# Performance work log

Hardware: AMD Instinct MI355X
Metric: run time of the kernel (lower is better)

## Reference

```python
import jax, jax.numpy as jnp
import numpy as np

B, IMG, TXT, N, FF, HID, C, E = 1024, 512, 300, 14, 2048, 128, 14, 182
D = IMG + TXT  # 812, transformer d_model


def setup_inputs() -> dict:
    key = jax.random.key(0)
    ks = jax.random.split(key, 12)
    r = lambda k, s, sc=0.02: (jax.random.normal(k, s, jnp.float32) * sc)
    return {
        "img_feat": jax.random.normal(ks[0], (B, IMG), jnp.float32),
        "word_embeds": jax.random.normal(ks[1], (N, TXT), jnp.float32),
        "edge_index": jax.random.randint(ks[2], (2, E), 0, N, jnp.int32),
        "in_proj_w": r(ks[3], (3 * D, D)),
        "in_proj_b": jnp.zeros((3 * D,), jnp.float32),
        "out_proj_w": r(ks[4], (D, D)),
        "out_proj_b": jnp.zeros((D,), jnp.float32),
        "ln1_g": jnp.ones((D,), jnp.float32), "ln1_b": jnp.zeros((D,), jnp.float32),
        "ln2_g": jnp.ones((D,), jnp.float32), "ln2_b": jnp.zeros((D,), jnp.float32),
        "ffn_w1": r(ks[5], (D, FF)), "ffn_b1": jnp.zeros((FF,), jnp.float32),
        "ffn_w2": r(ks[6], (FF, D)), "ffn_b2": jnp.zeros((D,), jnp.float32),
        "gcn1_w": r(ks[7], (D, HID)), "gcn1_b": jnp.zeros((HID,), jnp.float32),
        "gcn2_w": r(ks[8], (HID, HID)), "gcn2_b": jnp.zeros((HID,), jnp.float32),
        "lin_w": r(ks[9], (HID, C)), "lin_b": jnp.zeros((C,), jnp.float32),
    }


def layer_norm(x, g, b, eps=1e-5):
    mu = x.mean(-1, keepdims=True)
    var = ((x - mu) ** 2).mean(-1, keepdims=True)
    return (x - mu) * jax.lax.rsqrt(var + eps) * g + b


def gcn_conv(x, edge_index, W, b, n_nodes):
    # PyG GCNConv: add self loops, symmetric normalization, x @ W then scatter-add.
    # x: (B, N, F_in); gather/scatter along node axis (node_dim=-2).
    src, dst = edge_index[0], edge_index[1]
    loop = jnp.arange(n_nodes, dtype=src.dtype)
    src = jnp.concatenate([src, loop])
    dst = jnp.concatenate([dst, loop])
    deg = jnp.zeros((n_nodes,), x.dtype).at[dst].add(1.0)
    dinv = jnp.where(deg > 0, deg ** -0.5, 0.0)
    ew = dinv[src] * dinv[dst]                       # (E+N,)
    h = x @ W                                        # (B, N, F_out)
    msg = h[:, src, :] * ew[None, :, None]           # gather neighbors
    out = jnp.zeros_like(h).at[:, dst, :].add(msg)   # scatter-aggregate
    return out + b


def reference(img_feat, word_embeds, edge_index,
              in_proj_w, in_proj_b, out_proj_w, out_proj_b,
              ln1_g, ln1_b, ln2_g, ln2_b,
              ffn_w1, ffn_b1, ffn_w2, ffn_b2,
              gcn1_w, gcn1_b, gcn2_w, gcn2_b, lin_w, lin_b):
    # Broadcast image feature across the 14 label nodes; concat word embeddings.
    node = jnp.concatenate([
        jnp.broadcast_to(img_feat[:, None, :], (B, N, IMG)),
        jnp.broadcast_to(word_embeds[None, :, :], (B, N, TXT)),
    ], axis=-1)                                      # (B, N, D)

    # torch TransformerEncoderLayer, batch_first=False, nhead=1, post-norm, relu.
    # Input (B, N, D) is interpreted as (seq=B, batch=N, D): attention over dim 0.
    qkv = node @ in_proj_w.T + in_proj_b
    q, k, v = jnp.split(qkv, 3, axis=-1)             # each (B, N, D)
    scale = 1.0 / jnp.sqrt(jnp.asarray(D, node.dtype))
    scores = jnp.einsum('lnd,mnd->nlm', q, k) * scale  # (N, B, B)
    attn = jax.nn.softmax(scores, axis=-1)
    ao = jnp.einsum('nlm,mnd->lnd', attn, v)           # (B, N, D)
    ao = ao @ out_proj_w.T + out_proj_b
    x = layer_norm(node + ao, ln1_g, ln1_b)
    ff = jax.nn.relu(x @ ffn_w1 + ffn_b1) @ ffn_w2 + ffn_b2
    x = layer_norm(x + ff, ln2_g, ln2_b)               # (B, N, D)

    # Two GCNConv layers over the 14-node label graph (batched over B).
    x = jax.nn.relu(gcn_conv(x, edge_index, gcn1_w, gcn1_b, N))
    x = gcn_conv(x, edge_index, gcn2_w, gcn2_b, N)
    x = jax.nn.relu(x.mean(axis=1))                    # mean over nodes -> (B, HID)
    return x @ lin_w + lin_b                           # (B, C)
```

## Files before the change

### kernel.cpp

```cpp
#include <hip/hip_runtime.h>
#include <math.h>

#define B_    1024
#define IMG_  512
#define TXT_  300
#define NN_   14
#define FF_   2048
#define HID_  128
#define CC_   14
#define EE_   182
#define DD_   812
#define D3_   2436
#define BNR_  14336
#define KP_   832
#define TXP_  320
#define AROWS_ 1152

typedef __bf16 bf16x8 __attribute__((ext_vector_type(8)));
typedef float  f32x4  __attribute__((ext_vector_type(4)));
typedef unsigned short u16;

__device__ __forceinline__ u16 f2bf(float f) {
    union { float f; unsigned u; } v; v.f = f;
    unsigned r = v.u + 0x7FFFu + ((v.u >> 16) & 1u);
    return (u16)(r >> 16);
}
__device__ __forceinline__ float bf2f(u16 h) {
    union { unsigned u; float f; } v; v.u = ((unsigned)h) << 16; return v.f;
}

__device__ __forceinline__ void gload_lds16(const u16* g, u16* l) {
    __builtin_amdgcn_global_load_lds(
        (const __attribute__((address_space(1))) void*)g,
        (__attribute__((address_space(3))) void*)l, 16, 0, 0);
}

#define OFF_IMGB  0ULL
#define OFF_WIB   1048576ULL
#define OFF_WORDB 3543040ULL
#define OFF_WITX  3624960ULL
#define OFF_GB    0ULL
#define OFF_EBUF  29360128ULL
#define OFF_AVOT  33611776ULL
#define OFF_WOB   35446784ULL
#define OFF_HB    0ULL
#define OFF_PB    58720256ULL
#define OFF_X1B   82001920ULL
#define OFF_YB    105857024ULL
#define OFF_W1T   129712128ULL
#define OFF_W2T   133120000ULL
#define OFF_AQB   152420352ULL
#define OFF_TVB   158307552ULL
#define OFF_CO    158520544ULL
#define OFF_Z     158566016ULL
#define OFF_ADJ   158623360ULL
#define OFF_WG1T  158624384ULL
#define OFF_WG2T  158837376ULL

__device__ __forceinline__ void gemm_epi(
    float v, int rm, int cn, int epi,
    float* __restrict__ Cf, int ldc, u16* __restrict__ Cb, int ldcb,
    const float* __restrict__ bias)
{
    if (epi == 0) Cf[(size_t)rm * ldc + cn] = v;
    else if (epi == 1) { v += bias[cn]; v = v > 0.f ? v : 0.f;
                    Cb[(size_t)rm * ldcb + cn] = f2bf(v); }
    else if (epi == 2) Cf[(size_t)rm * ldc + cn] =
                    v + bias[cn] + bf2f(Cb[(size_t)rm * ldcb + cn]);
    else if (epi == 3) Cb[(size_t)rm * ldcb + cn] = f2bf(v);
    else if (epi == 4) { int bs = cn / DD_, cc = cn - bs * DD_;
                    Cb[(size_t)bs * (AROWS_ * KP_) + (size_t)rm * KP_ + cc] = f2bf(v); }
    else if (epi == 5) { float invz = 1.0f / bias[rm];
                    Cb[(size_t)rm * ldcb + cn] = f2bf(v * invz); }
    else if (epi == 6) Cf[(size_t)rm * ldc + cn] = v + bias[cn];
    else if (epi == 7) { const u16* rx = (const u16*)Cf;
                    Cb[(size_t)rm * ldcb + cn] =
                        f2bf(v + bias[cn] + bf2f(rx[(size_t)rm * ldc + cn])); }
    else if (epi == 8) {
        float t = v + bias[cn];
        if (cn < DD_) Cb[(size_t)(1024 + rm) * KP_ + cn] = f2bf(t);
        else if (cn >= 2 * DD_)
            ((u16*)Cf)[(size_t)rm * KP_ + (cn - 2 * DD_)] = f2bf(t);
    }
}

__device__ __forceinline__ void gemm_body4(
    const u16* __restrict__ A, int lda,
    const u16* __restrict__ Bm, int ldb,
    int M, int N, int K, float scale,
    float* __restrict__ Cf, int ldc,
    u16* __restrict__ Cb, int ldcb,
    const float* __restrict__ bias,
    int nxt, int swiz, int epi, int id)
{
    __shared__ __align__(16) u16 As[2][128 * 32];
    __shared__ __align__(16) u16 Bs[2][128 * 32];
    const int tid = threadIdx.x;
    int bx, by;
    if (swiz) { int r8 = id & 7; int q = id >> 3; bx = q % nxt; by = (q / nxt) * 8 + r8; }
    else      { bx = id % nxt; by = id / nxt; }
    const int row0 = by * 128, col0 = bx * 128;
    const int lane = tid & 63, wv = tid >> 6;
    const int wm = (wv >> 1) * 64, wn = (wv & 1) * 64;
    const int fr = lane & 15, qd = lane >> 4;

    const int s_r0  = (wv * 64 + lane) >> 2;
    const int s_sw  = ((lane & 3) ^ ((lane >> 3) & 3)) * 8;
    const int s_b0  = (wv * 64) * 8;
    const u16* Arow0 = A  + (size_t)(row0 + s_r0) * lda + s_sw;
    const u16* Arow1 = A  + (size_t)(row0 + s_r0 + 64) * lda + s_sw;
    const u16* Brow0 = Bm + (size_t)(col0 + s_r0) * ldb + s_sw;
    const u16* Brow1 = Bm + (size_t)(col0 + s_r0 + 64) * ldb + s_sw;
    const int qsw = (qd ^ ((fr >> 1) & 3)) * 8;

    f32x4 acc[4][4] = {};

    const int T = K >> 5;
    gload_lds16(Arow0, &As[0][s_b0]);
    gload_lds16(Arow1, &As[0][s_b0 + 2048]);
    gload_lds16(Brow0, &Bs[0][s_b0]);
    gload_lds16(Brow1, &Bs[0][s_b0 + 2048]);

    for (int i = 0; i < T; ++i) {
        __syncthreads();
        const int cur = i & 1;
        if (i + 1 < T) {
            const int nb = cur ^ 1;
            const int ko = (i + 1) << 5;
            gload_lds16(Arow0 + ko, &As[nb][s_b0]);
            gload_lds16(Arow1 + ko, &As[nb][s_b0 + 2048]);
            gload_lds16(Brow0 + ko, &Bs[nb][s_b0]);
            gload_lds16(Brow1 + ko, &Bs[nb][s_b0 + 2048]);
        }
        bf16x8 af[4], bg[4];
        #pragma unroll
        for (int j = 0; j < 4; ++j) {
            af[j] = *(const bf16x8*)&As[cur][(wm + j * 16 + fr) * 32 + qsw];
            bg[j] = *(const bf16x8*)&Bs[cur][(wn + j * 16 + fr) * 32 + qsw];
        }
        #pragma unroll
        for (int mi = 0; mi < 4; ++mi)
            #pragma unroll
            for (int ni = 0; ni < 4; ++ni)
                acc[mi][ni] = __builtin_amdgcn_mfma_f32_16x16x32_bf16(
                    af[mi], bg[ni], acc[mi][ni], 0, 0, 0);
    }

    #pragma unroll
    for (int mi = 0; mi < 4; ++mi) {
        #pragma unroll
        for (int i = 0; i < 4; ++i) {
            int rm = row0 + wm + mi * 16 + qd * 4 + i;
            if (rm >= M) continue;
            #pragma unroll
            for (int ni = 0; ni < 4; ++ni) {
                int cn = col0 + wn + ni * 16 + fr;
                if (cn >= N) continue;
                gemm_epi(acc[mi][ni][i] * scale, rm, cn, epi, Cf, ldc, Cb, ldcb, bias);
            }
        }
    }
}

template<int EPI>
__global__ __launch_bounds__(256, 4)
void bgemm(const u16* __restrict__ A, int lda,
           const u16* __restrict__ Bm, int ldb,
           int M, int N, int K, float scale,
           float* __restrict__ Cf, int ldc,
           u16* __restrict__ Cb, int ldcb,
           const float* __restrict__ bias,
           int nxt, int swiz)
{
    gemm_body4(A, lda, Bm, ldb, M, N, K, scale, Cf, ldc, Cb, ldcb, bias,
               nxt, swiz, EPI, blockIdx.x);
}

__device__ __forceinline__ void gemm256_body(
    const u16* __restrict__ A, int lda,
    const u16* __restrict__ Bm, int ldb,
    int M, int N, int K, float scale,
    float* __restrict__ Cf, int ldc,
    u16* __restrict__ Cb, int ldcb,
    const float* __restrict__ bias,
    int nxt, int epi, int id)
{
    __shared__ __align__(16) u16 As[4][8192];
    __shared__ __align__(16) u16 Bs[4][8192];
    const int tid = threadIdx.x;
    const int bx = id % nxt, by = id / nxt;
    const int row0 = by << 8, col0 = bx << 8;
    const int lane = tid & 63, wv = tid >> 6;
    const int wm = (wv >> 2) << 7;
    const int wn = (wv & 3) << 6;
    const int fr = lane & 15, qd = lane >> 4;

    int aoff[8], boff[4];
    #pragma unroll
    for (int mi = 0; mi < 8; ++mi) {
        int r = wm + mi * 16 + fr;
        aoff[mi] = r * 32 + ((qd ^ ((r >> 1) & 3)) << 3);
    }
    #pragma unroll
    for (int ni = 0; ni < 4; ++ni) {
        int r = wn + ni * 16 + fr;
        boff[ni] = r * 32 + ((qd ^ ((r >> 1) & 3)) << 3);
    }

    const int i0 = tid, i1 = 512 + tid;
    const int r0 = i0 >> 2, r1 = i1 >> 2;
    const int c0 = ((i0 & 3) ^ ((r0 >> 1) & 3)) << 3;
    const int c1 = ((i1 & 3) ^ ((r1 >> 1) & 3)) << 3;
    const u16* Ag0 = A  + (size_t)(row0 + r0) * lda + c0;
    const u16* Ag1 = A  + (size_t)(row0 + r1) * lda + c1;
    const u16* Bg0 = Bm + (size_t)(col0 + r0) * ldb + c0;
    const u16* Bg1 = Bm + (size_t)(col0 + r1) * ldb + c1;
    const int lb0 = wv * 512;
    const int lb1 = 4096 + wv * 512;

    f32x4 acc[8][4] = {};
    const int T = K >> 5;

    #pragma unroll
    for (int p = 0; p < 3; ++p) {
        const int ko = p << 5;
        gload_lds16(Ag0 + ko, &As[p][lb0]);
        gload_lds16(Ag1 + ko, &As[p][lb1]);
        gload_lds16(Bg0 + ko, &Bs[p][lb0]);
        gload_lds16(Bg1 + ko, &Bs[p][lb1]);
    }
    __builtin_amdgcn_sched_barrier(0);
    asm volatile("s_waitcnt vmcnt(8)");
    __builtin_amdgcn_sched_barrier(0);
    __builtin_amdgcn_s_barrier();
    __builtin_amdgcn_sched_barrier(0);

    for (int t = 0; t < T; ++t) {
        const int slot = t & 3;
        const u16* as = &As[slot][0];
        const u16* bs = &Bs[slot][0];
        const int ns = (t + 3) & 3;
        const int ko = (t + 3) << 5;
        const bool pf = (t + 3 < T);

        bf16x8 a[8];
        #pragma unroll
        for (int mi = 0; mi < 8; ++mi)
            a[mi] = *(const bf16x8*)(as + aoff[mi]);
        bf16x8 b0 = *(const bf16x8*)(bs + boff[0]);
        bf16x8 b1 = *(const bf16x8*)(bs + boff[1]);
        if (pf) {
            gload_lds16(Ag0 + ko, &As[ns][lb0]);
            gload_lds16(Ag1 + ko, &As[ns][lb1]);
        }
        __builtin_amdgcn_sched_barrier(0);
        __builtin_amdgcn_s_barrier();
        __builtin_amdgcn_sched_barrier(0);
        __builtin_amdgcn_s_setprio(1);
        #pragma unroll
        for (int mi = 0; mi < 8; ++mi) {
            acc[mi][0] = __builtin_amdgcn_mfma_f32_16x16x32_bf16(
                a[mi], b0, acc[mi][0], 0, 0, 0);
            acc[mi][1] = __builtin_amdgcn_mfma_f32_16x16x32_bf16(
                a[mi], b1, acc[mi][1], 0, 0, 0);
        }
        __builtin_amdgcn_s_setprio(0);
        __builtin_amdgcn_sched_barrier(0);
        __builtin_amdgcn_s_barrier();
        __builtin_amdgcn_sched_barrier(0);

        bf16x8 b2 = *(const bf16x8*)(bs + boff[2]);
        bf16x8 b3 = *(const bf16x8*)(bs + boff[3]);
        if (pf) {
            gload_lds16(Bg0 + ko, &Bs[ns][lb0]);
            gload_lds16(Bg1 + ko, &Bs[ns][lb1]);
        }
        __builtin_amdgcn_sched_barrier(0);
        if (t < T - 3) asm volatile("s_waitcnt vmcnt(8)");
        else           asm volatile("s_waitcnt vmcnt(0)");
        __builtin_amdgcn_sched_barrier(0);
        __builtin_amdgcn_s_barrier();
        __builtin_amdgcn_sched_barrier(0);
        __builtin_amdgcn_s_setprio(1);
        #pragma unroll
        for (int mi = 0; mi < 8; ++mi) {
            acc[mi][2] = __builtin_amdgcn_mfma_f32_16x16x32_bf16(
                a[mi], b2, acc[mi][2], 0, 0, 0);
            acc[mi][3] = __builtin_amdgcn_mfma_f32_16x16x32_bf16(
                a[mi], b3, acc[mi][3], 0, 0, 0);
        }
        __builtin_amdgcn_s_setprio(0);
        __builtin_amdgcn_sched_barrier(0);
        __builtin_amdgcn_s_barrier();
        __builtin_amdgcn_sched_barrier(0);
    }

    #pragma unroll
    for (int mi = 0; mi < 8; ++mi) {
        #pragma unroll
        for (int i = 0; i < 4; ++i) {
            int rm = row0 + wm + mi * 16 + qd * 4 + i;
            if (rm >= M) continue;
            #pragma unroll
            for (int ni = 0; ni < 4; ++ni) {
                int cn = col0 + wn + ni * 16 + fr;
                if (cn >= N) continue;
                gemm_epi(acc[mi][ni][i] * scale, rm, cn, epi, Cf, ldc, Cb, ldcb, bias);
            }
        }
    }
}

template<int EPI>
__global__ __launch_bounds__(512, 2)
void bgemm256(const u16* __restrict__ A, int lda,
              const u16* __restrict__ Bm, int ldb,
              int M, int N, int K, float scale,
              float* __restrict__ Cf, int ldc,
              u16* __restrict__ Cb, int ldcb,
              const float* __restrict__ bias,
              int nxt)
{
    const int g8 = (int)gridDim.x >> 3;
    const int id = (int)blockIdx.x;
    const int w = (id & 7) * g8 + (id >> 3);
    gemm256_body(A, lda, Bm, ldb, M, N, K, scale, Cf, ldc, Cb, ldcb, bias,
                 nxt, EPI, w);
}

__device__ __forceinline__ void gemm_body8(
    const u16* __restrict__ A, int lda,
    const u16* __restrict__ Bm, int ldb,
    int M, int N, int K, float scale,
    float* __restrict__ Cf, int ldc,
    u16* __restrict__ Cb, int ldcb,
    const float* __restrict__ bias,
    int nxt, int swiz, int epi, int id)
{
    __shared__ __align__(16) u16 As[2][128 * 32];
    __shared__ __align__(16) u16 Bs[2][128 * 32];
    const int tid = threadIdx.x;
    int bx, by;
    if (swiz) { int r8 = id & 7; int q = id >> 3; bx = q % nxt; by = (q / nxt) * 8 + r8; }
    else      { bx = id % nxt; by = id / nxt; }
    const int row0 = by * 128, col0 = bx * 128;
    const int lane = tid & 63, wv = tid >> 6;
    const int wm = (wv >> 1) * 32, wn = (wv & 1) * 64;
    const int fr = lane & 15, qd = lane >> 4;

    const int s_b0  = wv * 512;
    const int s_row = tid >> 2;
    const int s_sw  = ((tid & 3) ^ ((tid >> 3) & 3)) * 8;
    const u16* Arow = A  + (size_t)(row0 + s_row) * lda + s_sw;
    const u16* Brow = Bm + (size_t)(col0 + s_row) * ldb + s_sw;
    const int qsw = (qd ^ ((fr >> 1) & 3)) * 8;

    f32x4 acc[2][4] = {};

    const int T = K >> 5;
    gload_lds16(Arow, &As[0][s_b0]);
    gload_lds16(Brow, &Bs[0][s_b0]);

    for (int i = 0; i < T; ++i) {
        __syncthreads();
        const int cur = i & 1;
        if (i + 1 < T) {
            const int ko = (i + 1) << 5;
            gload_lds16(Arow + ko, &As[cur ^ 1][s_b0]);
            gload_lds16(Brow + ko, &Bs[cur ^ 1][s_b0]);
        }
        bf16x8 af[2], bg[4];
        #pragma unroll
        for (int j = 0; j < 2; ++j)
            af[j] = *(const bf16x8*)&As[cur][(wm + j * 16 + fr) * 32 + qsw];
        #pragma unroll
        for (int j = 0; j < 4; ++j)
            bg[j] = *(const bf16x8*)&Bs[cur][(wn + j * 16 + fr) * 32 + qsw];
        #pragma unroll
        for (int mi = 0; mi < 2; ++mi)
            #pragma unroll
            for (int ni = 0; ni < 4; ++ni)
                acc[mi][ni] = __builtin_amdgcn_mfma_f32_16x16x32_bf16(
                    af[mi], bg[ni], acc[mi][ni], 0, 0, 0);
    }

    #pragma unroll
    for (int mi = 0; mi < 2; ++mi) {
        #pragma unroll
        for (int i = 0; i < 4; ++i) {
            int rm = row0 + wm + mi * 16 + qd * 4 + i;
            if (rm >= M) continue;
            #pragma unroll
            for (int ni = 0; ni < 4; ++ni) {
                int cn = col0 + wn + ni * 16 + fr;
                if (cn >= N) continue;
                gemm_epi(acc[mi][ni][i] * scale, rm, cn, epi, Cf, ldc, Cb, ldcb, bias);
            }
        }
    }
}

struct GDesc {
    const u16* A; const u16* B; float* Cf; u16* Cb; const float* bias;
    int lda, ldb, ldc, ldcb, M, N, K, epi, nxt, swiz, blk0;
    float scale;
};
struct TDesc { const float* src; u16* dst; int srs, drs, rows, cols, padrows, rt, nblk; };
struct MPack { GDesc g[3]; TDesc t[2]; const int* ei; float* Adj; int ng, gtot, nt; };

__device__ __forceinline__ void castT_body(TDesc T, int id)
{
    __shared__ float t[32][33];
    const int bx = id % T.rt, by = id / T.rt;
    const int r0 = bx * 32, c0 = by * 32;
    const int tx = threadIdx.x & 31, ty = threadIdx.x >> 5;
    #pragma unroll
    for (int k = 0; k < 2; ++k) {
        int r = r0 + ty + k * 16, c = c0 + tx;
        t[ty + k * 16][tx] = (r < T.rows && c < T.cols) ? T.src[(size_t)r * T.srs + c] : 0.f;
    }
    __syncthreads();
    #pragma unroll
    for (int k = 0; k < 2; ++k) {
        int c = c0 + ty + k * 16, r = r0 + tx;
        if (c < T.cols && r < T.padrows)
            T.dst[(size_t)c * T.drs + r] = f2bf(t[tx][ty + k * 16]);
    }
}

__device__ __forceinline__ void adj_body(const int* __restrict__ ei, float* __restrict__ Adj)
{
    __shared__ float degS[NN_], dinvS[NN_], adjS[NN_ * NN_];
    const int tid = threadIdx.x;
    if (tid < NN_) degS[tid] = 1.f;
    if (tid < NN_ * NN_) adjS[tid] = 0.f;
    __syncthreads();
    int s = 0, d = 0;
    if (tid < EE_) { s = ei[tid]; d = ei[EE_ + tid]; atomicAdd(&degS[d], 1.f); }
    __syncthreads();
    if (tid < NN_) dinvS[tid] = rsqrtf(degS[tid]);
    __syncthreads();
    if (tid < EE_) atomicAdd(&adjS[d * NN_ + s], dinvS[s] * dinvS[d]);
    if (tid < NN_) atomicAdd(&adjS[tid * NN_ + tid], dinvS[tid] * dinvS[tid]);
    __syncthreads();
    if (tid < NN_ * NN_) Adj[tid] = adjS[tid];
    if (tid < 16) {
        float sum = 0.f;
        if (tid < NN_)
            for (int j = 0; j < NN_; ++j) sum += adjS[j * NN_ + tid];
        Adj[NN_ * NN_ + tid] = sum / (float)NN_;
    }
}

__global__ __launch_bounds__(512, 6)
void kern_mix(MPack p)
{
    int id = blockIdx.x;
    if (id < p.gtot) {
        int si = 0;
        for (int s = 1; s < p.ng; ++s) if (id >= p.g[s].blk0) si = s;
        GDesc D = p.g[si];
        gemm_body8(D.A, D.lda, D.B, D.ldb, D.M, D.N, D.K, D.scale,
                   D.Cf, D.ldc, D.Cb, D.ldcb, D.bias, D.nxt, D.swiz, D.epi,
                   id - D.blk0);
        return;
    }
    id -= p.gtot;
    for (int s = 0; s < p.nt; ++s) {
        if (id < p.t[s].nblk) { castT_body(p.t[s], id); return; }
        id -= p.t[s].nblk;
    }
    if (id == 0 && p.ei) adj_body(p.ei, p.Adj);
}

struct CDesc { const float* src; u16* dst; int srs, drs, dcols, scols; };
struct CPack { CDesc d[9]; unsigned cum[10]; int n; };

__global__ void kern_mcast(CPack p)
{
    unsigned idx = blockIdx.x * 256 + threadIdx.x;
    int si = -1;
    for (int s = 0; s < p.n; ++s)
        if (idx >= p.cum[s] && idx < p.cum[s + 1]) { si = s; break; }
    if (si < 0) return;
    CDesc D = p.d[si];
    unsigned k = idx - p.cum[si];
    int r = k / D.dcols, c = k - r * D.dcols;
    D.dst[(size_t)r * D.drs + c] =
        (c < D.scols) ? f2bf(D.src[(size_t)r * D.srs + c]) : (u16)0;
}

__global__ __launch_bounds__(256) void kern_eG(const float* __restrict__ S,
    u16* __restrict__ Gb, float* __restrict__ Z)
{
    __shared__ float red[256];
    __shared__ u16 ews[NN_ * 1024];
    const int l = blockIdx.x, tid = threadIdx.x;
    const int lane = tid & 63, wv = tid >> 6;

    const float* wraw = S + 1024 * 1024;
    for (int z = wv; z < NN_; z += 4) {
        const float* r = wraw + z * 1024;
        float vv[16], mx = -1e30f;
        #pragma unroll
        for (int j = 0; j < 16; ++j) { vv[j] = r[lane + 64 * j]; mx = fmaxf(mx, vv[j]); }
        #pragma unroll
        for (int off = 32; off > 0; off >>= 1) mx = fmaxf(mx, __shfl_down(mx, off));
        mx = __shfl(mx, 0);
        #pragma unroll
        for (int j = 0; j < 16; ++j)
            ews[z * 1024 + lane + 64 * j] = f2bf(expf(vv[j] - mx));
    }
    const float* row = S + (size_t)l * 1024;
    float m = -1e30f;
    #pragma unroll
    for (int k = 0; k < 4; ++k) m = fmaxf(m, row[tid + 256 * k]);
    red[tid] = m; __syncthreads();
    for (int s = 128; s > 0; s >>= 1) {
        if (tid < s) red[tid] = fmaxf(red[tid], red[tid + s]);
        __syncthreads();
    }
    m = red[0];
    float ev[16];
    #pragma unroll
    for (int j = 0; j < 16; ++j) ev[j] = expf(row[lane + 64 * j] - m);
    u16* gr = Gb + (size_t)l * NN_ * 1024;
    for (int z = wv; z < NN_; z += 4) {
        const u16* er = &ews[z * 1024];
        float s = 0.f;
        #pragma unroll
        for (int j = 0; j < 16; ++j) {
            float pv = ev[j] * bf2f(er[lane + 64 * j]);
            gr[(size_t)z * 1024 + lane + 64 * j] = f2bf(pv);
            s += pv;
        }
        #pragma unroll
        for (int off = 32; off > 0; off >>= 1) s += __shfl_down(s, off);
        if (lane == 0) Z[l * NN_ + z] = s;
    }
}

__global__ __launch_bounds__(256) void kern_ln1(
    const float* __restrict__ img, const float* __restrict__ word,
    const u16* __restrict__ Pb,
    const float* __restrict__ co, const float* __restrict__ g,
    const float* __restrict__ bta, u16* __restrict__ Xb)
{
    __shared__ float buf[DD_];
    __shared__ float red[256];
    __shared__ float stats[2];
    int row = blockIdx.x;
    int b = row / NN_, n = row - b * NN_;
    const u16* pr = Pb + (size_t)row * DD_;
    const float* cr = co + n * DD_;
    float s = 0.f;
    for (int d = threadIdx.x; d < DD_; d += 256) {
        float v = (d < IMG_) ? img[(size_t)b * IMG_ + d] : word[n * TXT_ + d - IMG_];
        v += bf2f(pr[d]) + cr[d];
        buf[d] = v; s += v;
    }
    red[threadIdx.x] = s; __syncthreads();
    for (int t = 128; t > 0; t >>= 1) {
        if (threadIdx.x < t) red[threadIdx.x] += red[threadIdx.x + t];
        __syncthreads();
    }
    if (threadIdx.x == 0) stats[0] = red[0] / DD_;
    __syncthreads();
    float mu = stats[0], s2 = 0.f;
    for (int d = threadIdx.x; d < DD_; d += 256) { float t = buf[d] - mu; s2 += t * t; }
    red[threadIdx.x] = s2; __syncthreads();
    for (int t = 128; t > 0; t >>= 1) {
        if (threadIdx.x < t) red[threadIdx.x] += red[threadIdx.x + t];
        __syncthreads();
    }
    if (threadIdx.x == 0) stats[1] = rsqrtf(red[0] / DD_ + 1e-5f);
    __syncthreads();
    float rstd = stats[1];
    u16* xb = Xb + (size_t)row * KP_;
    for (int d = threadIdx.x; d < DD_; d += 256)
        xb[d] = f2bf((buf[d] - mu) * rstd * g[d] + bta[d]);
    for (int d = DD_ + threadIdx.x; d < KP_; d += 256) xb[d] = 0;
}

#define X2S_ 840
#define G1S_ 136
__global__ __launch_bounds__(256, 4)
void kern_gcn(const u16* __restrict__ Yb,
              const float* __restrict__ g2v, const float* __restrict__ bt2,
              const u16* __restrict__ Wg1T, const float* __restrict__ bg1,
              const u16* __restrict__ Wg2T, const float* __restrict__ bg2,
              const float* __restrict__ Wl,  const float* __restrict__ bl,
              const float* __restrict__ AdjW, float* __restrict__ out)
{
    __shared__ __align__(16) u16 x2s[16 * X2S_];
    __shared__ __align__(16) float h1s[16 * 132];
    __shared__ float adj_s[NN_ * NN_];
    __shared__ float colw_s[16];
    __shared__ float pool_s[HID_];
    u16* g1s = x2s;
    const int b = blockIdx.x, tid = threadIdx.x;
    const int lane = tid & 63, wv = tid >> 6;
    const int fr = lane & 15, qd = lane >> 4;

    if (tid < NN_ * NN_) adj_s[tid] = AdjW[tid];
    if (tid >= NN_ * NN_ && tid < NN_ * NN_ + 16) colw_s[tid - NN_ * NN_] = AdjW[tid];
    for (int k = tid; k < 2 * X2S_; k += 256) x2s[14 * X2S_ + k] = 0;
    for (int k = tid; k < 14 * (X2S_ - DD_); k += 256) {
        int j = k / (X2S_ - DD_), c = k - j * (X2S_ - DD_);
        x2s[j * X2S_ + DD_ + c] = 0;
    }

    for (int j = wv; j < NN_; j += 4) {
        const u16* yr = Yb + (size_t)(b * NN_ + j) * KP_;
        float vv[13], s = 0.f;
        #pragma unroll
        for (int k = 0; k < 13; ++k) {
            int d = lane + 64 * k;
            float v = (d < DD_) ? bf2f(yr[d]) : 0.f;
            vv[k] = v; s += v;
        }
        #pragma unroll
        for (int off = 32; off > 0; off >>= 1) s += __shfl_down(s, off);
        s = __shfl(s, 0);
        float mu = s / (float)DD_, s2 = 0.f;
        #pragma unroll
        for (int k = 0; k < 13; ++k) {
            int d = lane + 64 * k;
            float t = (d < DD_) ? vv[k] - mu : 0.f;
            s2 += t * t;
        }
        #pragma unroll
        for (int off = 32; off > 0; off >>= 1) s2 += __shfl_down(s2, off);
        s2 = __shfl(s2, 0);
        float rstd = rsqrtf(s2 / (float)DD_ + 1e-5f);
        #pragma unroll
        for (int k = 0; k < 13; ++k) {
            int d = lane + 64 * k;
            if (d < DD_)
                x2s[j * X2S_ + d] = f2bf((vv[k] - mu) * rstd * g2v[d] + bt2[d]);
        }
    }
    __syncthreads();

    {
        f32x4 acc[2] = {{}, {}};
        const u16* wp0 = Wg1T + (size_t)(wv * 32 + fr) * KP_ + qd * 8;
        const u16* wp1 = wp0 + (size_t)16 * KP_;
        bf16x8 bc0 = *(const bf16x8*)wp0;
        bf16x8 bc1 = *(const bf16x8*)wp1;
        for (int k0 = 0; k0 < KP_; k0 += 32) {
            bf16x8 bn0 = bc0, bn1 = bc1;
            if (k0 + 32 < KP_) {
                bn0 = *(const bf16x8*)(wp0 + k0 + 32);
                bn1 = *(const bf16x8*)(wp1 + k0 + 32);
            }
            bf16x8 af = *(const bf16x8*)&x2s[fr * X2S_ + k0 + qd * 8];
            acc[0] = __builtin_amdgcn_mfma_f32_16x16x32_bf16(af, bc0, acc[0], 0, 0, 0);
            acc[1] = __builtin_amdgcn_mfma_f32_16x16x32_bf16(af, bc1, acc[1], 0, 0, 0);
            bc0 = bn0; bc1 = bn1;
        }
        #pragma unroll
        for (int t = 0; t < 2; ++t)
            #pragma unroll
            for (int i = 0; i < 4; ++i)
                h1s[(qd * 4 + i) * 132 + wv * 32 + t * 16 + fr] = acc[t][i];
    }
    __syncthreads();

    {
        const int f = tid & 127, jj = (tid >> 7) * 7;
        #pragma unroll
        for (int j = 0; j < 7; ++j) {
            float s = bg1[f];
            #pragma unroll
            for (int i = 0; i < NN_; ++i)
                s = fmaf(adj_s[(jj + j) * NN_ + i], h1s[i * 132 + f], s);
            g1s[(jj + j) * G1S_ + f] = f2bf(s > 0.f ? s : 0.f);
        }
        for (int k = tid; k < 2 * G1S_; k += 256) g1s[14 * G1S_ + k] = 0;
    }
    __syncthreads();

    {
        f32x4 acc[2] = {{}, {}};
        const u16* wp0 = Wg2T + (size_t)(wv * 32 + fr) * HID_ + qd * 8;
        const u16* wp1 = wp0 + (size_t)16 * HID_;
        bf16x8 bc0 = *(const bf16x8*)wp0;
        bf16x8 bc1 = *(const bf16x8*)wp1;
        for (int k0 = 0; k0 < HID_; k0 += 32) {
            bf16x8 bn0 = bc0, bn1 = bc1;
            if (k0 + 32 < HID_) {
                bn0 = *(const bf16x8*)(wp0 + k0 + 32);
                bn1 = *(const bf16x8*)(wp1 + k0 + 32);
            }
            bf16x8 af = *(const bf16x8*)&g1s[fr * G1S_ + k0 + qd * 8];
            acc[0] = __builtin_amdgcn_mfma_f32_16x16x32_bf16(af, bc0, acc[0], 0, 0, 0);
            acc[1] = __builtin_amdgcn_mfma_f32_16x16x32_bf16(af, bc1, acc[1], 0, 0, 0);
            bc0 = bn0; bc1 = bn1;
        }
        #pragma unroll
        for (int t = 0; t < 2; ++t) {
            float s = 0.f;
            #pragma unroll
            for (int i = 0; i < 4; ++i) s += colw_s[qd * 4 + i] * acc[t][i];
            s += __shfl_xor(s, 16);
            s += __shfl_xor(s, 32);
            if (qd == 0) {
                int f = wv * 32 + t * 16 + fr;
                float p = s + bg2[f];
                pool_s[f] = p > 0.f ? p : 0.f;
            }
        }
    }
    __syncthreads();

    if (tid < CC_) {
        float s = bl[tid];
        #pragma unroll 8
        for (int f = 0; f < HID_; ++f)
            s = fmaf(pool_s[f], Wl[(size_t)f * CC_ + tid], s);
        out[(size_t)b * CC_ + tid] = s;
    }
}

extern "C" void kernel_launch(void* const* d_in, const int* in_sizes, int n_in,
                              void* d_out, int out_size, void* d_ws, size_t ws_size,
                              hipStream_t stream)
{
    const float* img  = (const float*)d_in[0];
    const float* word = (const float*)d_in[1];
    const int*   ei   = (const int*)d_in[2];
    const float* Wi   = (const float*)d_in[3];
    const float* bi   = (const float*)d_in[4];
    const float* Wo   = (const float*)d_in[5];
    const float* bo   = (const float*)d_in[6];
    const float* g1   = (const float*)d_in[7];
    const float* bt1  = (const float*)d_in[8];
    const float* g2   = (const float*)d_in[9];
    const float* bt2  = (const float*)d_in[10];
    const float* W1   = (const float*)d_in[11];
    const float* bf1  = (const float*)d_in[12];
    const float* W2   = (const float*)d_in[13];
    const float* bf2  = (const float*)d_in[14];
    const float* Wg1  = (const float*)d_in[15];
    const float* bg1  = (const float*)d_in[16];
    const float* Wg2  = (const float*)d_in[17];
    const float* bg2  = (const float*)d_in[18];
    const float* Wl   = (const float*)d_in[19];
    const float* bl   = (const float*)d_in[20];
    float* out = (float*)d_out;

    char* ws = (char*)d_ws;
    u16*   imgb = (u16*)  (ws + OFF_IMGB);
    u16*   Wib  = (u16*)  (ws + OFF_WIB);
    u16*   wordb= (u16*)  (ws + OFF_WORDB);
    u16*   WiTX = (u16*)  (ws + OFF_WITX);
    u16*   Gb   = (u16*)  (ws + OFF_GB);
    float* Ebuf = (float*)(ws + OFF_EBUF);
    u16*   AvoT = (u16*)  (ws + OFF_AVOT);
    u16*   Wob  = (u16*)  (ws + OFF_WOB);
    u16*   Hb   = (u16*)  (ws + OFF_HB);
    u16*   Pb   = (u16*)  (ws + OFF_PB);
    u16*   X1b  = (u16*)  (ws + OFF_X1B);
    u16*   Yb   = (u16*)  (ws + OFF_YB);
    u16*   W1T  = (u16*)  (ws + OFF_W1T);
    u16*   W2T  = (u16*)  (ws + OFF_W2T);
    u16*   Aqb  = (u16*)  (ws + OFF_AQB);
    u16*   Akb  = Aqb + AROWS_ * KP_;
    u16*   Avb  = Aqb + 2 * AROWS_ * KP_;
    u16*   Tvb  = (u16*)  (ws + OFF_TVB);
    float* co   = (float*)(ws + OFF_CO);
    float* Zb   = (float*)(ws + OFF_Z);
    float* Adj  = (float*)(ws + OFF_ADJ);
    u16*   Wg1T = (u16*)  (ws + OFF_WG1T);
    u16*   Wg2T = (u16*)  (ws + OFF_WG2T);

    const float scl = 1.0f / sqrtf((float)DD_);

    {
        CPack p; p.n = 9;
        unsigned c = 0;
        auto seg = [&](int i, const float* s, int srs, u16* d, int drs,
                       int rows, int dcols, int scols) {
            p.d[i] = { s, d, srs, drs, dcols, scols };
            p.cum[i] = c; c += (unsigned)rows * dcols;
        };
        seg(0, img,        IMG_, imgb,  IMG_, B_,   IMG_, IMG_);
        seg(1, Wi,         DD_,  Wib,   IMG_, D3_,  IMG_, IMG_);
        seg(2, word,       TXT_, wordb, TXP_, NN_,  TXP_, TXT_);
        seg(3, Wi + IMG_,  DD_,  WiTX,  TXP_, D3_,  TXP_, TXT_);
        seg(4, Wo,         DD_,  Wob,   KP_,  DD_,  KP_,  DD_);
        seg(5, nullptr, 0, Aqb + DD_,                    KP_, 1038, 20, 0);
        seg(6, nullptr, 0, Aqb + AROWS_ * KP_ + DD_,     KP_, 1024, 20, 0);
        seg(7, nullptr, 0, Aqb + 2 * AROWS_ * KP_ + DD_, KP_, 1024, 20, 0);
        seg(8, nullptr, 0, Tvb + DD_,                    KP_, NN_,  20, 0);
        p.cum[9] = c;
        kern_mcast<<<(c + 255) / 256, 256, 0, stream>>>(p);
    }

    {
        MPack p{};
        p.ng = 2; p.gtot = 180;
        p.g[0] = { wordb, WiTX, (float*)Tvb, Aqb, bi,
                   TXP_, TXP_, 0, 0, NN_, D3_, TXP_, 8, 20, 0, 0, 1.f };
        p.g[1] = { imgb, Wib, nullptr, Aqb, nullptr,
                   IMG_, IMG_, 0, 0, B_, D3_, IMG_, 4, 20, 1, 20, 1.f };
        p.nt = 2;
        p.t[0] = { Wg1, Wg1T, HID_, KP_,  DD_,  HID_, KP_,  26, 26 * 4 };
        p.t[1] = { Wg2, Wg2T, HID_, HID_, HID_, HID_, HID_, 4,  4 * 4 };
        p.ei = ei; p.Adj = Adj;
        kern_mix<<<180 + 104 + 16 + 1, 512, 0, stream>>>(p);
    }

    {
        MPack p{};
        p.ng = 3; p.gtot = 135;
        p.g[0] = { Aqb, Akb, Ebuf, nullptr, nullptr,
                   KP_, KP_, 1024, 0, 1024 + NN_, 1024, KP_, 0, 8, 0, 0, scl };
        p.g[1] = { Wob, Avb, nullptr, AvoT, nullptr,
                   KP_, KP_, 0, 1024, DD_, B_, KP_, 3, 8, 0, 72, 1.f };
        p.g[2] = { Tvb, Wob, co, nullptr, bo,
                   KP_, KP_, DD_, 0, NN_, DD_, KP_, 6, 7, 0, 128, 1.f };
        p.nt = 2;
        p.t[0] = { W1, W1T, FF_, KP_, DD_, FF_, KP_, 26, 26 * 64 };
        p.t[1] = { W2, W2T, DD_, FF_, FF_, DD_, FF_, 64, 64 * 26 };
        p.ei = nullptr; p.Adj = nullptr;
        kern_mix<<<135 + 1664 + 1664, 512, 0, stream>>>(p);
    }

    kern_eG<<<1024, 256, 0, stream>>>(Ebuf, Gb, Zb);

    bgemm<5><<<7 * 112, 256, 0, stream>>>(Gb, 1024, AvoT, 1024,
        BNR_, DD_, 1024, 1.f, nullptr, 0, Pb, DD_, Zb, 7, 1);

    kern_ln1<<<BNR_, 256, 0, stream>>>(img, word, Pb, co, g1, bt1, X1b);

    bgemm<1><<<16 * 112, 256, 0, stream>>>(X1b, KP_, W1T, KP_,
        BNR_, FF_, KP_, 1.f, nullptr, 0, Hb, FF_, bf1, 16, 1);

    bgemm256<7><<<56 * 4, 512, 0, stream>>>(Hb, FF_, W2T, FF_,
        BNR_, DD_, FF_, 1.f, (float*)X1b, KP_, Yb, KP_, bf2, 4);

    kern_gcn<<<B_, 256, 0, stream>>>(Yb, g2, bt2, Wg1T, bg1, Wg2T, bg2,
                                     Wl, bl, Adj, out);
}
```

Baseline: 457.4 us.

## Split-K across warp groups in mixed GEMM and vectorize LN1 kernel

```diff
diff --git a/kernel.cpp b/kernel.cpp
--- a/kernel.cpp
+++ b/kernel.cpp
@@ -19,6 +19,8 @@
 typedef __bf16 bf16x8 __attribute__((ext_vector_type(8)));
 typedef float  f32x4  __attribute__((ext_vector_type(4)));
 typedef unsigned short u16;
+typedef unsigned short u16x4 __attribute__((ext_vector_type(4)));
+typedef unsigned short u16x8 __attribute__((ext_vector_type(8)));
 
 __device__ __forceinline__ u16 f2bf(float f) {
     union { float f; unsigned u; } v; v.f = f;
@@ -337,64 +339,88 @@
     const float* __restrict__ bias,
     int nxt, int swiz, int epi, int id)
 {
-    __shared__ __align__(16) u16 As[2][128 * 32];
-    __shared__ __align__(16) u16 Bs[2][128 * 32];
+    __shared__ __align__(16) u16 As[2][2][128 * 32];
+    __shared__ __align__(16) u16 Bs[2][2][128 * 32];
     const int tid = threadIdx.x;
     int bx, by;
     if (swiz) { int r8 = id & 7; int q = id >> 3; bx = q % nxt; by = (q / nxt) * 8 + r8; }
     else      { bx = id % nxt; by = id / nxt; }
     const int row0 = by * 128, col0 = bx * 128;
     const int lane = tid & 63, wv = tid >> 6;
-    const int wm = (wv >> 1) * 32, wn = (wv & 1) * 64;
+    const int kg = wv >> 2;
+    const int ww = wv & 3;
+    const int wm = (ww >> 1) * 64, wn = (ww & 1) * 64;
     const int fr = lane & 15, qd = lane >> 4;
 
-    const int s_b0  = wv * 512;
-    const int s_row = tid >> 2;
-    const int s_sw  = ((tid & 3) ^ ((tid >> 3) & 3)) * 8;
-    const u16* Arow = A  + (size_t)(row0 + s_row) * lda + s_sw;
-    const u16* Brow = Bm + (size_t)(col0 + s_row) * ldb + s_sw;
+    const int r0   = ww * 16 + (lane >> 2);
+    const int s_sw = ((lane & 3) ^ ((lane >> 3) & 3)) * 8;
+    const u16* Ag0 = A  + (size_t)(row0 + r0) * lda + s_sw;
+    const u16* Ag1 = A  + (size_t)(row0 + r0 + 64) * lda + s_sw;
+    const u16* Bg0 = Bm + (size_t)(col0 + r0) * ldb + s_sw;
+    const u16* Bg1 = Bm + (size_t)(col0 + r0 + 64) * ldb + s_sw;
+    const int lb0 = ww * 512, lb1 = 2048 + ww * 512;
     const int qsw = (qd ^ ((fr >> 1) & 3)) * 8;
 
-    f32x4 acc[2][4] = {};
-
-    const int T = K >> 5;
-    gload_lds16(Arow, &As[0][s_b0]);
-    gload_lds16(Brow, &Bs[0][s_b0]);
-
-    for (int i = 0; i < T; ++i) {
+    f32x4 acc[4][4] = {};
+    const int Th = K >> 6;
+    const int kb = kg * Th;
+
+    gload_lds16(Ag0 + (kb << 5), &As[kg][0][lb0]);
+    gload_lds16(Ag1 + (kb << 5), &As[kg][0][lb1]);
+    gload_lds16(Bg0 + (kb << 5), &Bs[kg][0][lb0]);
+    gload_lds16(Bg1 + (kb << 5), &Bs[kg][0][lb1]);
+
+    for (int i = 0; i < Th; ++i) {
         __syncthreads();
         const int cur = i & 1;
-        if (i + 1 < T) {
-            const int ko = (i + 1) << 5;
-            gload_lds16(Arow + ko, &As[cur ^ 1][s_b0]);
-            gload_lds16(Brow + ko, &Bs[cur ^ 1][s_b0]);
-        }
-        bf16x8 af[2], bg[4];
-        #pragma unroll
-        for (int j = 0; j < 2; ++j)
-            af[j] = *(const bf16x8*)&As[cur][(wm + j * 16 + fr) * 32 + qsw];
-        #pragma unroll
-        for (int j = 0; j < 4; ++j)
-            bg[j] = *(const bf16x8*)&Bs[cur][(wn + j * 16 + fr) * 32 + qsw];
-        #pragma unroll
-        for (int mi = 0; mi < 2; ++mi)
+        if (i + 1 < Th) {
+            const int ko = (kb + i + 1) << 5;
+            gload_lds16(Ag0 + ko, &As[kg][cur ^ 1][lb0]);
+            gload_lds16(Ag1 + ko, &As[kg][cur ^ 1][lb1]);
+            gload_lds16(Bg0 + ko, &Bs[kg][cur ^ 1][lb0]);
+            gload_lds16(Bg1 + ko, &Bs[kg][cur ^ 1][lb1]);
+        }
+        bf16x8 af[4], bg[4];
+        #pragma unroll
+        for (int j = 0; j < 4; ++j) {
+            af[j] = *(const bf16x8*)&As[kg][cur][(wm + j * 16 + fr) * 32 + qsw];
+            bg[j] = *(const bf16x8*)&Bs[kg][cur][(wn + j * 16 + fr) * 32 + qsw];
+        }
+        #pragma unroll
+        for (int mi = 0; mi < 4; ++mi)
             #pragma unroll
             for (int ni = 0; ni < 4; ++ni)
                 acc[mi][ni] = __builtin_amdgcn_mfma_f32_16x16x32_bf16(
                     af[mi], bg[ni], acc[mi][ni], 0, 0, 0);
     }
 
-    #pragma unroll
-    for (int mi = 0; mi < 2; ++mi) {
-        #pragma unroll
-        for (int i = 0; i < 4; ++i) {
-            int rm = row0 + wm + mi * 16 + qd * 4 + i;
-            if (rm >= M) continue;
+    __syncthreads();
+    float* Cs = (wm == 0) ? (float*)As : (float*)Bs;
+    if (kg == 1) {
+        #pragma unroll
+        for (int mi = 0; mi < 4; ++mi)
             #pragma unroll
-            for (int ni = 0; ni < 4; ++ni) {
-                int cn = col0 + wn + ni * 16 + fr;
-                if (cn >= N) continue;
-                gemm_epi(acc[mi][ni][i] * scale, rm, cn, epi, Cf, ldc, Cb, ldcb, bias);
+            for (int i = 0; i < 4; ++i)
+                #pragma unroll
+                for (int ni = 0; ni < 4; ++ni)
+                    Cs[(mi * 16 + qd * 4 + i) * 128 + wn + ni * 16 + fr] =
+                        acc[mi][ni][i];
+    }
+    __syncthreads();
+    if (kg == 0) {
+        #pragma unroll
+        for (int mi = 0; mi < 4; ++mi) {
+            #pragma unroll
+            for (int i = 0; i < 4; ++i) {
+                int rm = row0 + wm + mi * 16 + qd * 4 + i;
+                #pragma unroll
+                for (int ni = 0; ni < 4; ++ni) {
+                    int cn = col0 + wn + ni * 16 + fr;
+                    float v = acc[mi][ni][i] +
+                        Cs[(mi * 16 + qd * 4 + i) * 128 + wn + ni * 16 + fr];
+                    if (rm < M && cn < N)
+                        gemm_epi(v * scale, rm, cn, epi, Cf, ldc, Cb, ldcb, bias);
+                }
             }
         }
     }
@@ -452,7 +478,7 @@
     }
 }
 
-__global__ __launch_bounds__(512, 6)
+__global__ __launch_bounds__(512, 4)
 void kern_mix(MPack p)
 {
     int id = blockIdx.x;
@@ -546,40 +572,62 @@
     const float* __restrict__ co, const float* __restrict__ g,
     const float* __restrict__ bta, u16* __restrict__ Xb)
 {
-    __shared__ float buf[DD_];
+    __shared__ float buf[816];
     __shared__ float red[256];
     __shared__ float stats[2];
     int row = blockIdx.x;
     int b = row / NN_, n = row - b * NN_;
     const u16* pr = Pb + (size_t)row * DD_;
     const float* cr = co + n * DD_;
+    const int t = threadIdx.x;
+    float v0 = 0.f, v1 = 0.f, v2 = 0.f, v3 = 0.f;
     float s = 0.f;
-    for (int d = threadIdx.x; d < DD_; d += 256) {
-        float v = (d < IMG_) ? img[(size_t)b * IMG_ + d] : word[n * TXT_ + d - IMG_];
-        v += bf2f(pr[d]) + cr[d];
-        buf[d] = v; s += v;
-    }
-    red[threadIdx.x] = s; __syncthreads();
-    for (int t = 128; t > 0; t >>= 1) {
-        if (threadIdx.x < t) red[threadIdx.x] += red[threadIdx.x + t];
+    if (t < 203) {
+        const int d = t * 4;
+        float4 iv = (d < IMG_) ? *(const float4*)&img[(size_t)b * IMG_ + d]
+                               : *(const float4*)&word[n * TXT_ + (d - IMG_)];
+        u16x4 pv = *(const u16x4*)&pr[d];
+        float4 cv = *(const float4*)&cr[d];
+        v0 = iv.x + bf2f(pv[0]) + cv.x;
+        v1 = iv.y + bf2f(pv[1]) + cv.y;
+        v2 = iv.z + bf2f(pv[2]) + cv.z;
+        v3 = iv.w + bf2f(pv[3]) + cv.w;
+        buf[d] = v0; buf[d + 1] = v1; buf[d + 2] = v2; buf[d + 3] = v3;
+        s = v0 + v1 + v2 + v3;
+    }
+    red[t] = s; __syncthreads();
+    for (int k = 128; k > 0; k >>= 1) {
+        if (t < k) red[t] += red[t + k];
         __syncthreads();
     }
-    if (threadIdx.x == 0) stats[0] = red[0] / DD_;
-    __syncthreads();
-    float mu = stats[0], s2 = 0.f;
-    for (int d = threadIdx.x; d < DD_; d += 256) { float t = buf[d] - mu; s2 += t * t; }
-    red[threadIdx.x] = s2; __syncthreads();
-    for (int t = 128; t > 0; t >>= 1) {
-        if (threadIdx.x < t) red[threadIdx.x] += red[threadIdx.x + t];
+    if (t == 0) stats[0] = red[0] / DD_;
+    __syncthreads();
+    float mu = stats[0];
+    float s2 = 0.f;
+    if (t < 203) {
+        float a0 = v0 - mu, a1 = v1 - mu, a2 = v2 - mu, a3 = v3 - mu;
+        s2 = a0 * a0 + a1 * a1 + a2 * a2 + a3 * a3;
+    }
+    red[t] = s2; __syncthreads();
+    for (int k = 128; k > 0; k >>= 1) {
+        if (t < k) red[t] += red[t + k];
         __syncthreads();
     }
-    if (threadIdx.x == 0) stats[1] = rsqrtf(red[0] / DD_ + 1e-5f);
+    if (t == 0) stats[1] = rsqrtf(red[0] / DD_ + 1e-5f);
     __syncthreads();
     float rstd = stats[1];
     u16* xb = Xb + (size_t)row * KP_;
-    for (int d = threadIdx.x; d < DD_; d += 256)
-        xb[d] = f2bf((buf[d] - mu) * rstd * g[d] + bta[d]);
-    for (int d = DD_ + threadIdx.x; d < KP_; d += 256) xb[d] = 0;
+    if (t < 104) {
+        const int d = t * 8;
+        u16x8 o;
+        #pragma unroll
+        for (int k = 0; k < 8; ++k) {
+            int dd = d + k;
+            o[k] = (dd < DD_)
+                 ? f2bf((buf[dd] - mu) * rstd * g[dd] + bta[dd]) : (u16)0;
+        }
+        *(u16x8*)&xb[d] = o;
+    }
 }
 
 #define X2S_ 840
```

After: 482.0 us. 1.05x slower.
